# Optimization experiments

Measured on AMD Instinct MI355X. Metric: run time of the kernel, lower is better.

## Reference

```python
import jax, jax.numpy as jnp
import numpy as np

# (npoint, radius, nsample) per SA stage, from module defaults
SA_CFG = [(2048, 0.2, 64), (1024, 0.4, 32), (512, 0.6, 16), (256, 1.2, 8)]


def fps(xyz, npoint):
    """Farthest point sampling, CUDA-kernel semantics: start at index 0.
    xyz: [B,N,3] -> idx [B,npoint] int32."""
    B, N, _ = xyz.shape

    def step(carry, _):
        dist, far = carry
        centroid = jnp.take_along_axis(xyz, far[:, None, None], axis=1)  # [B,1,3]
        d = jnp.sum((xyz - centroid) ** 2, axis=-1)                      # [B,N]
        dist = jnp.minimum(dist, d)
        return (dist, jnp.argmax(dist, axis=-1).astype(jnp.int32)), far

    init = (jnp.full((B, N), 1e10, xyz.dtype), jnp.zeros((B,), jnp.int32))
    _, idxs = jax.lax.scan(step, init, None, length=npoint)  # [npoint,B]
    return idxs.T


def gather(pts, idx):
    """pts: [B,N,C], idx: [B,...] int -> [B,...,C]."""
    return jax.vmap(lambda p, i: p[i])(pts, idx)


def ball_query(xyz, new_xyz, radius, nsample):
    """First-nsample-in-ball semantics of pointnet2 ball_query; pads with the
    first found neighbor. xyz:[B,N,3], new_xyz:[B,S,3] -> [B,S,nsample] int."""
    N = xyz.shape[1]
    # squared dists via ||a||^2 + ||b||^2 - 2ab to avoid a [B,S,N,3] temp
    d2 = (jnp.sum(new_xyz ** 2, -1)[:, :, None]
          + jnp.sum(xyz ** 2, -1)[:, None, :]
          - 2.0 * jnp.einsum('bsc,bnc->bsn', new_xyz, xyz))
    cand = jnp.where(d2 < radius * radius, jnp.arange(N)[None, None, :], N)
    idx = jnp.sort(cand, axis=-1)[..., :nsample]
    first = idx[..., :1]  # center itself is always in the ball (d2==0)
    return jnp.where(idx == N, first, idx)


def sa_stage(xyz, feats, npoint, radius, nsample, layers):
    """One PointnetSAModuleVotes: FPS + ball query + normalized relative xyz
    (use_xyz=True, normalize_xyz=True) + shared MLP + max pool over nsample."""
    fidx = fps(xyz, npoint)
    new_xyz = gather(xyz, fidx)                         # [B,S,3]
    nidx = ball_query(xyz, new_xyz, radius, nsample)    # [B,S,K]
    rel = (gather(xyz, nidx) - new_xyz[:, :, None, :]) / radius  # [B,S,K,3]
    x = rel if feats is None else jnp.concatenate([rel, gather(feats, nidx)], -1)
    for w, b in layers:  # shared 1x1-conv MLP (BN folded), ReLU
        x = jax.nn.relu(x @ w + b)
    return new_xyz, jnp.max(x, axis=2)                  # [B,S,C_out]


def setup_inputs() -> dict:
    key = jax.random.key(0)
    ks = jax.random.split(key, 16)
    inp = {"pointcloud": jax.random.normal(ks[0], (4, 16384, 3), jnp.float32)}
    dims = [(3, 64, 64, 128), (131, 128, 128, 256),
            (259, 256, 256, 512), (515, 512, 512, 512)]
    k = 1
    for s, d in enumerate(dims, 1):
        for l in range(3):
            inp[f"w{s}{l}"] = jax.random.normal(
                jax.random.fold_in(ks[k], l), (d[l], d[l + 1]), jnp.float32) * 0.02
            inp[f"b{s}{l}"] = jnp.zeros((d[l + 1],), jnp.float32)
        k += 1
    return inp


def reference(pointcloud,
              w10, b10, w11, b11, w12, b12,
              w20, b20, w21, b21, w22, b22,
              w30, b30, w31, b31, w32, b32,
              w40, b40, w41, b41, w42, b42):
    stage_params = [
        [(w10, b10), (w11, b11), (w12, b12)],
        [(w20, b20), (w21, b21), (w22, b22)],
        [(w30, b30), (w31, b31), (w32, b32)],
        [(w40, b40), (w41, b41), (w42, b42)],
    ]
    xyz = pointcloud[..., :3]
    feats = None  # input_feature_dim == 0
    for (npoint, radius, nsample), layers in zip(SA_CFG, stage_params):
        xyz, feats = sa_stage(xyz, feats, npoint, radius, nsample, layers)
    return xyz, feats  # sa4_xyz [B,256,3], sa4_features [B,256,512]
```

## Files before the change

### kernel.cpp

```cpp
#include <hip/hip_runtime.h>
#include <hip/hip_bf16.h>


#define B_SZ 4

typedef float v2f __attribute__((ext_vector_type(2)));
typedef unsigned long long u64;

__device__ __forceinline__ v2f pk_add(v2f a, v2f b) {
  v2f d;
  asm("v_pk_add_f32 %0, %1, %2" : "=v"(d) : "v"(a), "v"(b));
  return d;
}
__device__ __forceinline__ v2f pk_mul(v2f a, v2f b) {
  v2f d;
  asm("v_pk_mul_f32 %0, %1, %2" : "=v"(d) : "v"(a), "v"(b));
  return d;
}

template <int CTRL>
__device__ __forceinline__ u64 dpp_u64(u64 v) {
  int lo = (int)(unsigned)v;
  int hi = (int)(unsigned)(v >> 32);
  int nlo = __builtin_amdgcn_update_dpp(lo, lo, CTRL, 0xF, 0xF, false);
  int nhi = __builtin_amdgcn_update_dpp(hi, hi, CTRL, 0xF, 0xF, false);
  return ((u64)(unsigned)nhi << 32) | (unsigned)nlo;
}

__device__ __forceinline__ u64 wave_max_u64(u64 P) {
  u64 o;
  o = dpp_u64<0x111>(P); P = o > P ? o : P;
  o = dpp_u64<0x112>(P); P = o > P ? o : P;
  o = dpp_u64<0x114>(P); P = o > P ? o : P;
  o = dpp_u64<0x118>(P); P = o > P ? o : P;
  o = dpp_u64<0x142>(P); P = o > P ? o : P;
  o = dpp_u64<0x143>(P); P = o > P ? o : P;
  return P;
}

template <int N, int NPOINT, int T>
__global__ __launch_bounds__(T, 2) void fps1_kernel(const float* __restrict__ xyz,
                                                    int* __restrict__ fidx) {
#pragma clang fp contract(off)
  constexpr int PT = N / T;
  static_assert(PT % 2 == 0, "PT even");
  constexpr int NP2 = PT / 2;
  constexpr int NW = T / 64;
  constexpr int NACC = (NP2 >= 4) ? 4 : NP2;
  const int b = blockIdx.x;
  const int t = threadIdx.x;
  const int lane = t & 63;
  const int wv = t >> 6;
  const float* base = xyz + (size_t)b * N * 3;

  v2f px[NP2], py[NP2], pz[NP2], dv[NP2];
  __shared__ __align__(16) u64 s_key[2][NW];
  __shared__ float s_cx[2][NW], s_cy[2][NW], s_cz[2][NW];

#pragma unroll
  for (int j = 0; j < NP2; ++j) {
    int i0 = t + (2 * j) * T;
    int i1 = t + (2 * j + 1) * T;
    px[j][0] = base[i0 * 3 + 0]; py[j][0] = base[i0 * 3 + 1];
    pz[j][0] = base[i0 * 3 + 2];
    px[j][1] = base[i1 * 3 + 0]; py[j][1] = base[i1 * 3 + 1];
    pz[j][1] = base[i1 * 3 + 2];
    dv[j][0] = 1e10f; dv[j][1] = 1e10f;
  }

  int far = 0;
  float cenx = base[0], ceny = base[1], cenz = base[2];
  int p = 0;
  for (int it = 0; it < NPOINT; ++it) {
    if (t == 0) fidx[b * NPOINT + it] = far;
    const float nx = -cenx, ny = -ceny, nz = -cenz;
    const v2f c2x = {nx, nx}, c2y = {ny, ny}, c2z = {nz, nz};

    float mx[NACC];
#pragma unroll
    for (int q = 0; q < NACC; ++q) mx[q] = -1.0f;

#pragma unroll
    for (int j = 0; j < NP2; ++j) {
      v2f dx = pk_add(px[j], c2x);
      v2f dy = pk_add(py[j], c2y);
      v2f dz = pk_add(pz[j], c2z);
      v2f xx = pk_mul(dx, dx);
      v2f yy = pk_mul(dy, dy);
      v2f zz = pk_mul(dz, dz);
      v2f s = pk_add(xx, yy);
      v2f d = pk_add(s, zz);
      float nd0 = fminf(dv[j][0], d[0]);
      float nd1 = fminf(dv[j][1], d[1]);
      dv[j][0] = nd0; dv[j][1] = nd1;
      const int q = j % NACC;
      mx[q] = fmaxf(fmaxf(nd0, nd1), mx[q]);
    }
    float m = mx[0];
#pragma unroll
    for (int q = 1; q < NACC; ++q) m = fmaxf(m, mx[q]);

    int bk = 0;
#pragma unroll
    for (int j = NP2 - 1; j >= 0; --j) {
      if (dv[j][1] == m) bk = 2 * j + 1;
      if (dv[j][0] == m) bk = 2 * j;
    }

    int idx = t + bk * T;
    u64 P = ((u64)__float_as_uint(m) << 32) | (unsigned)(N - idx);
    P = wave_max_u64(P);

    int wf = N - __builtin_amdgcn_readlane((int)(unsigned)(P & 0xffffffffull), 63);
    float wx = base[wf * 3 + 0];
    float wy = base[wf * 3 + 1];
    float wz = base[wf * 3 + 2];
    if (lane == 63) s_key[p][wv] = P;
    if (lane == 0) { s_cx[p][wv] = wx; s_cy[p][wv] = wy; s_cz[p][wv] = wz; }
    __syncthreads();
    u64 bb = s_key[p][0];
    int mw = 0;
#pragma unroll
    for (int w = 1; w < NW; ++w) {
      u64 v = s_key[p][w];
      if (v > bb) { bb = v; mw = w; }
    }
    far = N - (int)(unsigned)(bb & 0xffffffffull);
    cenx = s_cx[p][mw]; ceny = s_cy[p][mw]; cenz = s_cz[p][mw];
    p ^= 1;
  }
}

template <int N, int NPOINT, int T>
__device__ __forceinline__ void fps_body_lds(char* smem,
                                             const float* __restrict__ xyz,
                                             int* __restrict__ fidx, int b) {
#pragma clang fp contract(off)
  constexpr int PT = N / T;
  static_assert(PT % 2 == 0, "PT even");
  constexpr int NP2 = PT / 2;
  constexpr int NW = T / 64;
  constexpr int NACC = (NP2 >= 4) ? 4 : NP2;
  u64* s_pack = (u64*)smem;
  float* s_x = (float*)(smem + 2 * NW * sizeof(u64));
  float* s_y = s_x + N;
  float* s_z = s_y + N;
  const int t = threadIdx.x;
  const int lane = t & 63;
  const int wv = t >> 6;
  const float* base = xyz + (size_t)b * N * 3;

  v2f px[NP2], py[NP2], pz[NP2], dv[NP2];
#pragma unroll
  for (int j = 0; j < NP2; ++j) {
    int i0 = t + (2 * j) * T;
    int i1 = t + (2 * j + 1) * T;
    px[j][0] = base[i0 * 3 + 0]; py[j][0] = base[i0 * 3 + 1];
    pz[j][0] = base[i0 * 3 + 2];
    px[j][1] = base[i1 * 3 + 0]; py[j][1] = base[i1 * 3 + 1];
    pz[j][1] = base[i1 * 3 + 2];
    dv[j][0] = 1e10f; dv[j][1] = 1e10f;
    s_x[i0] = px[j][0]; s_y[i0] = py[j][0]; s_z[i0] = pz[j][0];
    s_x[i1] = px[j][1]; s_y[i1] = py[j][1]; s_z[i1] = pz[j][1];
  }
  __syncthreads();

  int far = 0;
  int p = 0;
  for (int it = 0; it < NPOINT; ++it) {
    if (t == 0) fidx[b * NPOINT + it] = far;
    float cx = s_x[far], cy = s_y[far], cz = s_z[far];
    const float nx = -cx, ny = -cy, nz = -cz;
    const v2f c2x = {nx, nx}, c2y = {ny, ny}, c2z = {nz, nz};

    float mx[NACC];
#pragma unroll
    for (int q = 0; q < NACC; ++q) mx[q] = -1.0f;

#pragma unroll
    for (int j = 0; j < NP2; ++j) {
      v2f dx = pk_add(px[j], c2x);
      v2f dy = pk_add(py[j], c2y);
      v2f dz = pk_add(pz[j], c2z);
      v2f xx = pk_mul(dx, dx);
      v2f yy = pk_mul(dy, dy);
      v2f zz = pk_mul(dz, dz);
      v2f s = pk_add(xx, yy);
      v2f d = pk_add(s, zz);
      float nd0 = fminf(dv[j][0], d[0]);
      float nd1 = fminf(dv[j][1], d[1]);
      dv[j][0] = nd0; dv[j][1] = nd1;
      const int q = j % NACC;
      mx[q] = fmaxf(fmaxf(nd0, nd1), mx[q]);
    }
    float m = mx[0];
#pragma unroll
    for (int q = 1; q < NACC; ++q) m = fmaxf(m, mx[q]);

    int bk = 0;
#pragma unroll
    for (int j = NP2 - 1; j >= 0; --j) {
      if (dv[j][1] == m) bk = 2 * j + 1;
      if (dv[j][0] == m) bk = 2 * j;
    }

    int idx = t + bk * T;
    u64 P = ((u64)__float_as_uint(m) << 32) | (unsigned)(N - idx);
    P = wave_max_u64(P);
    if (lane == 63) s_pack[p * NW + wv] = P;
    __syncthreads();
    u64 bbp = s_pack[p * NW + 0];
#pragma unroll
    for (int w = 1; w < NW; ++w) {
      u64 v = s_pack[p * NW + w];
      bbp = v > bbp ? v : bbp;
    }
    far = N - (int)(unsigned)(bbp & 0xffffffffull);
    p ^= 1;
  }
}

__global__ void gather_xyz_kernel(const float* __restrict__ xyz,
                                  const int* __restrict__ fidx,
                                  float* __restrict__ out, int N, int S) {
  int s = blockIdx.x * blockDim.x + threadIdx.x;
  int b = blockIdx.y;
  if (s < S) {
    int i = fidx[b * S + s];
    out[((size_t)(b * S + s)) * 3 + 0] = xyz[((size_t)(b * N + i)) * 3 + 0];
    out[((size_t)(b * S + s)) * 3 + 1] = xyz[((size_t)(b * N + i)) * 3 + 1];
    out[((size_t)(b * S + s)) * 3 + 2] = xyz[((size_t)(b * N + i)) * 3 + 2];
  }
}

template <int N, int NS>
__global__ __launch_bounds__(256) void ball_query_kernel(
    const float* __restrict__ xyz, const float* __restrict__ new_xyz,
    int* __restrict__ nidx, int S, float r2) {
#pragma clang fp contract(off)
  const int wv = threadIdx.x >> 6;
  const int lane = threadIdx.x & 63;
  const int b = blockIdx.y;
  const int s = blockIdx.x * 4 + wv;
  __shared__ int s_idx[4][NS];
  const float* base = xyz + (size_t)b * N * 3;

  float cx = new_xyz[((size_t)(b * S + s)) * 3 + 0];
  float cy = new_xyz[((size_t)(b * S + s)) * 3 + 1];
  float cz = new_xyz[((size_t)(b * S + s)) * 3 + 2];
  float sc = (cx * cx + cy * cy) + cz * cz;

  int found = 0;
  for (int i0 = 0; i0 < N && found < NS; i0 += 64) {
    int i = i0 + lane;
    float x = base[i * 3 + 0];
    float y = base[i * 3 + 1];
    float z = base[i * 3 + 2];
    float sx = (x * x + y * y) + z * z;
    float dt = (cx * x + cy * y) + cz * z;
    float d2 = (sc + sx) - 2.0f * dt;
    bool inb = d2 < r2;
    unsigned long long m = __ballot(inb);
    if (inb) {
      int pos = found + __popcll(m & ((1ull << lane) - 1));
      if (pos < NS) s_idx[wv][pos] = i;
    }
    found += __popcll(m);
  }
  __syncthreads();
  int fcnt = found < NS ? found : NS;
  int first = s_idx[wv][0];
  int* outp = nidx + ((size_t)(b * S + s)) * NS;
  for (int j = lane; j < NS; j += 64) outp[j] = (j < fcnt) ? s_idx[wv][j] : first;
}

template <int R, int RG, int CG, int CMAXP, int CIN, int COUT>
__device__ __forceinline__ void mlp_layer(float* act, const float* __restrict__ w,
                                          const float* __restrict__ bias, int tid) {
  constexpr int RPT = R / RG;
  constexpr int CPT = COUT / CG;
  static_assert(RG * CG == 256, "thread grid");
  const int rg = tid / CG;
  const int cg = tid % CG;

  float acc[RPT][CPT];
#pragma unroll
  for (int rr = 0; rr < RPT; ++rr)
#pragma unroll
    for (int cc = 0; cc < CPT; ++cc) acc[rr][cc] = 0.f;

  constexpr int K4 = (CIN / 4) * 4;
  for (int k = 0; k < K4; k += 4) {
    float4 a[RPT];
#pragma unroll
    for (int rr = 0; rr < RPT; ++rr)
      a[rr] = *(const float4*)(&act[(rg * RPT + rr) * CMAXP + k]);
    float wvv[4][CPT];
#pragma unroll
    for (int kk = 0; kk < 4; ++kk)
#pragma unroll
      for (int cc = 0; cc < CPT; ++cc)
        wvv[kk][cc] = w[(size_t)(k + kk) * COUT + cg + cc * CG];
#pragma unroll
    for (int rr = 0; rr < RPT; ++rr) {
      float4 av = a[rr];
#pragma unroll
      for (int cc = 0; cc < CPT; ++cc) {
        acc[rr][cc] += av.x * wvv[0][cc];
        acc[rr][cc] += av.y * wvv[1][cc];
        acc[rr][cc] += av.z * wvv[2][cc];
        acc[rr][cc] += av.w * wvv[3][cc];
      }
    }
  }
#pragma unroll 1
  for (int k = K4; k < CIN; ++k) {
    float wvv[CPT];
#pragma unroll
    for (int cc = 0; cc < CPT; ++cc) wvv[cc] = w[(size_t)k * COUT + cg + cc * CG];
#pragma unroll
    for (int rr = 0; rr < RPT; ++rr) {
      float av = act[(rg * RPT + rr) * CMAXP + k];
#pragma unroll
      for (int cc = 0; cc < CPT; ++cc) acc[rr][cc] += av * wvv[cc];
    }
  }
  __syncthreads();
#pragma unroll
  for (int rr = 0; rr < RPT; ++rr)
#pragma unroll
    for (int cc = 0; cc < CPT; ++cc) {
      int co = cg + cc * CG;
      float v = acc[rr][cc] + bias[co];
      act[(rg * RPT + rr) * CMAXP + co] = fmaxf(v, 0.f);
    }
  __syncthreads();
}

template <int NS, int G, int CPREV, int CO0, int CO1, int CO2, int RG, int CG, int CMAXP>
__device__ __forceinline__ void group_mlp_body(
    char* smem, const float* __restrict__ xyz, const float* __restrict__ new_xyz,
    const float* __restrict__ feats, const int* __restrict__ nidx,
    const float* __restrict__ w0, const float* __restrict__ b0,
    const float* __restrict__ w1, const float* __restrict__ b1,
    const float* __restrict__ w2, const float* __restrict__ b2,
    float* __restrict__ out, int N, int S, float radius, int sblk, int b) {
  constexpr int R = NS * G;
  constexpr int CIN = 3 + CPREV;
  float* act = (float*)smem;
  const int tid = threadIdx.x;
  const int s0 = sblk * G;

  for (int i = tid; i < R * CIN; i += 256) {
    int row = i / CIN;
    int ch = i - row * CIN;
    int g = row / NS;
    int j = row - g * NS;
    int sidx = s0 + g;
    int n = nidx[((size_t)(b * S + sidx)) * NS + j];
    float v;
    if constexpr (CPREV == 0) {
      v = (xyz[((size_t)(b * N + n)) * 3 + ch] -
           new_xyz[((size_t)(b * S + sidx)) * 3 + ch]) /
          radius;
    } else {
      if (ch < 3) {
        v = (xyz[((size_t)(b * N + n)) * 3 + ch] -
             new_xyz[((size_t)(b * S + sidx)) * 3 + ch]) /
            radius;
      } else {
        v = feats[((size_t)(b * N + n)) * CPREV + (ch - 3)];
      }
    }
    act[row * CMAXP + ch] = v;
  }
  __syncthreads();

  mlp_layer<R, RG, CG, CMAXP, CIN, CO0>(act, w0, b0, tid);
  mlp_layer<R, RG, CG, CMAXP, CO0, CO1>(act, w1, b1, tid);
  mlp_layer<R, RG, CG, CMAXP, CO1, CO2>(act, w2, b2, tid);

  for (int i = tid; i < G * CO2; i += 256) {
    int g = i / CO2;
    int co = i - g * CO2;
    float m = act[(g * NS) * CMAXP + co];
    for (int j = 1; j < NS; ++j) m = fmaxf(m, act[(g * NS + j) * CMAXP + co]);
    out[((size_t)(b * S + s0 + g)) * CO2 + co] = m;
  }
}

template <int NS, int G, int CPREV, int CO0, int CO1, int CO2, int RG, int CG, int CMAXP>
__global__ __launch_bounds__(256, 4) void group_mlp_kernel(
    const float* __restrict__ xyz, const float* __restrict__ new_xyz,
    const float* __restrict__ feats, const int* __restrict__ nidx,
    const float* __restrict__ w0, const float* __restrict__ b0,
    const float* __restrict__ w1, const float* __restrict__ b1,
    const float* __restrict__ w2, const float* __restrict__ b2,
    float* __restrict__ out, int N, int S, float radius) {
  __shared__ __align__(16) char smem[NS * G * CMAXP * 4];
  group_mlp_body<NS, G, CPREV, CO0, CO1, CO2, RG, CG, CMAXP>(
      smem, xyz, new_xyz, feats, nidx, w0, b0, w1, b1, w2, b2, out, N, S,
      radius, blockIdx.x, blockIdx.y);
}

template <int FN, int FNP, int FT, int NS, int G, int CPREV, int CO0, int CO1,
          int CO2, int RG, int CG, int CMAXP>
__global__ __launch_bounds__(256, 4) void fused_fps_mlp_kernel(
    const float* __restrict__ fpts, int* __restrict__ fidx,
    const float* __restrict__ xyz, const float* __restrict__ new_xyz,
    const float* __restrict__ feats, const int* __restrict__ nidx,
    const float* __restrict__ w0, const float* __restrict__ b0,
    const float* __restrict__ w1, const float* __restrict__ b1,
    const float* __restrict__ w2, const float* __restrict__ b2,
    float* __restrict__ out, int N, int S, float radius, int SBLK) {
  constexpr int FPS_B = 2 * (FT / 64) * (int)sizeof(u64) + 3 * FN * 4;
  constexpr int MLP_B = NS * G * CMAXP * 4;
  constexpr int SB = (FPS_B > MLP_B) ? FPS_B : MLP_B;
  __shared__ __align__(16) char smem[SB];
  if ((int)blockIdx.x < B_SZ) {
    __builtin_amdgcn_s_setprio(1);
    fps_body_lds<FN, FNP, FT>(smem, fpts, fidx, blockIdx.x);
    __builtin_amdgcn_s_setprio(0);
  } else {
    int bid = (int)blockIdx.x - B_SZ;
    group_mlp_body<NS, G, CPREV, CO0, CO1, CO2, RG, CG, CMAXP>(
        smem, xyz, new_xyz, feats, nidx, w0, b0, w1, b1, w2, b2, out, N, S,
        radius, bid % SBLK, bid / SBLK);
  }
}

extern "C" void kernel_launch(void* const* d_in, const int* in_sizes, int n_in,
                              void* d_out, int out_size, void* d_ws, size_t ws_size,
                              hipStream_t stream) {
  (void)in_sizes; (void)n_in; (void)out_size; (void)ws_size;
  const float* pc = (const float*)d_in[0];
  const float* W[4][3];
  const float* Bb[4][3];
  for (int s = 0; s < 4; ++s)
    for (int l = 0; l < 3; ++l) {
      W[s][l] = (const float*)d_in[1 + s * 6 + l * 2];
      Bb[s][l] = (const float*)d_in[2 + s * 6 + l * 2];
    }

  char* wsp = (char*)d_ws;
  int* fidx = (int*)wsp;
  int* nidx = (int*)(wsp + (32 << 10));
  float* xyzA = (float*)(wsp + (32 << 10) + (2 << 20));
  float* xyzB = xyzA + B_SZ * 2048 * 3;
  float* featA = xyzB + B_SZ * 2048 * 3;
  float* featB = featA + B_SZ * 2048 * 128;
  float* oxyz = (float*)d_out;
  float* ofeat = oxyz + B_SZ * 256 * 3;

  hipLaunchKernelGGL((fps1_kernel<16384, 2048, 512>), dim3(B_SZ), dim3(512), 0, stream,
                     pc, fidx);
  hipLaunchKernelGGL(gather_xyz_kernel, dim3(32, B_SZ), dim3(64), 0, stream,
                     pc, fidx, xyzA, 16384, 2048);
  hipLaunchKernelGGL((ball_query_kernel<16384, 64>), dim3(512, B_SZ), dim3(256), 0, stream,
                     pc, xyzA, nidx, 2048, (float)(0.2 * 0.2));

  hipLaunchKernelGGL((fused_fps_mlp_kernel<2048, 1024, 256,
                                           64, 1, 0, 64, 64, 128, 8, 32, 128>),
                     dim3(B_SZ + 2048 * B_SZ), dim3(256), 0, stream,
                     xyzA, fidx,
                     pc, xyzA, (const float*)nullptr, nidx,
                     W[0][0], Bb[0][0], W[0][1], Bb[0][1], W[0][2], Bb[0][2],
                     featA, 16384, 2048, 0.2f, 2048);
  hipLaunchKernelGGL(gather_xyz_kernel, dim3(16, B_SZ), dim3(64), 0, stream,
                     xyzA, fidx, xyzB, 2048, 1024);
  hipLaunchKernelGGL((ball_query_kernel<2048, 32>), dim3(256, B_SZ), dim3(256), 0, stream,
                     xyzA, xyzB, nidx, 1024, (float)(0.4 * 0.4));

  hipLaunchKernelGGL((fused_fps_mlp_kernel<1024, 512, 256,
                                           32, 1, 128, 128, 128, 256, 4, 64, 256>),
                     dim3(B_SZ + 1024 * B_SZ), dim3(256), 0, stream,
                     xyzB, fidx,
                     xyzA, xyzB, featA, nidx,
                     W[1][0], Bb[1][0], W[1][1], Bb[1][1], W[1][2], Bb[1][2],
                     featB, 2048, 1024, 0.4f, 1024);
  hipLaunchKernelGGL(gather_xyz_kernel, dim3(8, B_SZ), dim3(64), 0, stream,
                     xyzB, fidx, xyzA, 1024, 512);
  hipLaunchKernelGGL((ball_query_kernel<1024, 16>), dim3(128, B_SZ), dim3(256), 0, stream,
                     xyzB, xyzA, nidx, 512, (float)(0.6 * 0.6));

  hipLaunchKernelGGL((fused_fps_mlp_kernel<512, 256, 256,
                                           16, 1, 256, 256, 256, 512, 2, 128, 512>),
                     dim3(B_SZ + 512 * B_SZ), dim3(256), 0, stream,
                     xyzA, fidx,
                     xyzB, xyzA, featB, nidx,
                     W[2][0], Bb[2][0], W[2][1], Bb[2][1], W[2][2], Bb[2][2],
                     featA, 1024, 512, 0.6f, 512);
  hipLaunchKernelGGL(gather_xyz_kernel, dim3(4, B_SZ), dim3(64), 0, stream,
                     xyzA, fidx, oxyz, 512, 256);
  hipLaunchKernelGGL((ball_query_kernel<512, 8>), dim3(64, B_SZ), dim3(256), 0, stream,
                     xyzA, oxyz, nidx, 256, (float)(1.2 * 1.2));

  hipLaunchKernelGGL((group_mlp_kernel<8, 2, 512, 512, 512, 512, 2, 128, 516>),
                     dim3(128, B_SZ), dim3(256), 0, stream,
                     xyzA, oxyz, featA, nidx,
                     W[3][0], Bb[3][0], W[3][1], Bb[3][1], W[3][2], Bb[3][2],
                     ofeat, 512, 256, 1.2f);
}
```

Baseline: 5.031 ms.

## Run stage 2-4 FPS in a single wave without block barriers

The later-stage FPS loops, which share a kernel with the grouped MLP, now run on one 64-lane wave instead of a 256-thread block. Each iteration finishes with a wave-level DPP reduction and a readlane, with no __syncthreads or LDS exchange. Points are kept in LDS as float4 so the next centroid comes from one load. The stage-1 FPS now fetches the winning centroid from global memory after the block reduction instead of passing per-wave candidates through LDS, and the index rescan is split into independent chunks. The trade is more registers and serial work per lane in the single-wave version, plus a dependent global load per iteration in stage 1.

```diff
diff --git a/kernel.cpp b/kernel.cpp
--- a/kernel.cpp
+++ b/kernel.cpp
@@ -38,15 +38,68 @@
   return P;
 }
 
+template <int NP2>
+__device__ __forceinline__ float upd_pts(const v2f* px, const v2f* py,
+                                         const v2f* pz, v2f* dv, float cx,
+                                         float cy, float cz) {
+#pragma clang fp contract(off)
+  constexpr int NACC = (NP2 >= 4) ? 4 : NP2;
+  const float nx = -cx, ny = -cy, nz = -cz;
+  const v2f c2x = {nx, nx}, c2y = {ny, ny}, c2z = {nz, nz};
+  float mx[NACC];
+#pragma unroll
+  for (int q = 0; q < NACC; ++q) mx[q] = -1.0f;
+#pragma unroll
+  for (int j = 0; j < NP2; ++j) {
+    v2f dx = pk_add(px[j], c2x);
+    v2f dy = pk_add(py[j], c2y);
+    v2f dz = pk_add(pz[j], c2z);
+    v2f xx = pk_mul(dx, dx);
+    v2f yy = pk_mul(dy, dy);
+    v2f zz = pk_mul(dz, dz);
+    v2f s = pk_add(xx, yy);
+    v2f d = pk_add(s, zz);
+    float nd0 = fminf(dv[j][0], d[0]);
+    float nd1 = fminf(dv[j][1], d[1]);
+    dv[j][0] = nd0; dv[j][1] = nd1;
+    const int q = j % NACC;
+    mx[q] = fmaxf(fmaxf(nd0, nd1), mx[q]);
+  }
+  float m = mx[0];
+#pragma unroll
+  for (int q = 1; q < NACC; ++q) m = fmaxf(m, mx[q]);
+  return m;
+}
+
+template <int NP2>
+__device__ __forceinline__ int rescan_idx(const v2f* dv, float m) {
+  constexpr int NCH = (NP2 >= 4) ? 4 : NP2;
+  constexpr int CL = NP2 / NCH;
+  int bkq[NCH];
+#pragma unroll
+  for (int q = 0; q < NCH; ++q) {
+    int bk = 0x7fffffff;
+#pragma unroll
+    for (int jj = CL - 1; jj >= 0; --jj) {
+      int j = q * CL + jj;
+      if (dv[j][1] == m) bk = 2 * j + 1;
+      if (dv[j][0] == m) bk = 2 * j;
+    }
+    bkq[q] = bk;
+  }
+  int bk = bkq[NCH - 1];
+#pragma unroll
+  for (int q = NCH - 2; q >= 0; --q) bk = (bkq[q] != 0x7fffffff) ? bkq[q] : bk;
+  return bk;
+}
+
 template <int N, int NPOINT, int T>
 __global__ __launch_bounds__(T, 2) void fps1_kernel(const float* __restrict__ xyz,
                                                     int* __restrict__ fidx) {
 #pragma clang fp contract(off)
   constexpr int PT = N / T;
-  static_assert(PT % 2 == 0, "PT even");
   constexpr int NP2 = PT / 2;
   constexpr int NW = T / 64;
-  constexpr int NACC = (NP2 >= 4) ? 4 : NP2;
   const int b = blockIdx.x;
   const int t = threadIdx.x;
   const int lane = t & 63;
@@ -54,8 +107,7 @@
   const float* base = xyz + (size_t)b * N * 3;
 
   v2f px[NP2], py[NP2], pz[NP2], dv[NP2];
-  __shared__ __align__(16) u64 s_key[2][NW];
-  __shared__ float s_cx[2][NW], s_cy[2][NW], s_cz[2][NW];
+  __shared__ __align__(16) u64 s_pack[2][NW];
 
 #pragma unroll
   for (int j = 0; j < NP2; ++j) {
@@ -73,150 +125,64 @@
   int p = 0;
   for (int it = 0; it < NPOINT; ++it) {
     if (t == 0) fidx[b * NPOINT + it] = far;
-    const float nx = -cenx, ny = -ceny, nz = -cenz;
-    const v2f c2x = {nx, nx}, c2y = {ny, ny}, c2z = {nz, nz};
-
-    float mx[NACC];
-#pragma unroll
-    for (int q = 0; q < NACC; ++q) mx[q] = -1.0f;
-
-#pragma unroll
-    for (int j = 0; j < NP2; ++j) {
-      v2f dx = pk_add(px[j], c2x);
-      v2f dy = pk_add(py[j], c2y);
-      v2f dz = pk_add(pz[j], c2z);
-      v2f xx = pk_mul(dx, dx);
-      v2f yy = pk_mul(dy, dy);
-      v2f zz = pk_mul(dz, dz);
-      v2f s = pk_add(xx, yy);
-      v2f d = pk_add(s, zz);
-      float nd0 = fminf(dv[j][0], d[0]);
-      float nd1 = fminf(dv[j][1], d[1]);
-      dv[j][0] = nd0; dv[j][1] = nd1;
-      const int q = j % NACC;
-      mx[q] = fmaxf(fmaxf(nd0, nd1), mx[q]);
-    }
-    float m = mx[0];
-#pragma unroll
-    for (int q = 1; q < NACC; ++q) m = fmaxf(m, mx[q]);
-
-    int bk = 0;
-#pragma unroll
-    for (int j = NP2 - 1; j >= 0; --j) {
-      if (dv[j][1] == m) bk = 2 * j + 1;
-      if (dv[j][0] == m) bk = 2 * j;
-    }
-
+    float m = upd_pts<NP2>(px, py, pz, dv, cenx, ceny, cenz);
+    int bk = rescan_idx<NP2>(dv, m);
     int idx = t + bk * T;
     u64 P = ((u64)__float_as_uint(m) << 32) | (unsigned)(N - idx);
     P = wave_max_u64(P);
-
-    int wf = N - __builtin_amdgcn_readlane((int)(unsigned)(P & 0xffffffffull), 63);
-    float wx = base[wf * 3 + 0];
-    float wy = base[wf * 3 + 1];
-    float wz = base[wf * 3 + 2];
-    if (lane == 63) s_key[p][wv] = P;
-    if (lane == 0) { s_cx[p][wv] = wx; s_cy[p][wv] = wy; s_cz[p][wv] = wz; }
+    if (lane == 63) s_pack[p][wv] = P;
     __syncthreads();
-    u64 bb = s_key[p][0];
-    int mw = 0;
+    u64 bb = s_pack[p][0];
 #pragma unroll
     for (int w = 1; w < NW; ++w) {
-      u64 v = s_key[p][w];
-      if (v > bb) { bb = v; mw = w; }
+      u64 v = s_pack[p][w];
+      bb = v > bb ? v : bb;
     }
     far = N - (int)(unsigned)(bb & 0xffffffffull);
-    cenx = s_cx[p][mw]; ceny = s_cy[p][mw]; cenz = s_cz[p][mw];
+    cenx = base[far * 3 + 0];
+    ceny = base[far * 3 + 1];
+    cenz = base[far * 3 + 2];
     p ^= 1;
   }
 }
 
-template <int N, int NPOINT, int T>
-__device__ __forceinline__ void fps_body_lds(char* smem,
-                                             const float* __restrict__ xyz,
-                                             int* __restrict__ fidx, int b) {
+template <int N, int NPOINT>
+__device__ __forceinline__ void fps_wave_body(char* smem,
+                                              const float* __restrict__ xyz,
+                                              int* __restrict__ fidx, int b) {
 #pragma clang fp contract(off)
-  constexpr int PT = N / T;
-  static_assert(PT % 2 == 0, "PT even");
+  constexpr int PT = N / 64;
   constexpr int NP2 = PT / 2;
-  constexpr int NW = T / 64;
-  constexpr int NACC = (NP2 >= 4) ? 4 : NP2;
-  u64* s_pack = (u64*)smem;
-  float* s_x = (float*)(smem + 2 * NW * sizeof(u64));
-  float* s_y = s_x + N;
-  float* s_z = s_y + N;
-  const int t = threadIdx.x;
-  const int lane = t & 63;
-  const int wv = t >> 6;
+  float4* s_p = (float4*)smem;
+  const int lane = threadIdx.x & 63;
   const float* base = xyz + (size_t)b * N * 3;
 
   v2f px[NP2], py[NP2], pz[NP2], dv[NP2];
 #pragma unroll
   for (int j = 0; j < NP2; ++j) {
-    int i0 = t + (2 * j) * T;
-    int i1 = t + (2 * j + 1) * T;
-    px[j][0] = base[i0 * 3 + 0]; py[j][0] = base[i0 * 3 + 1];
-    pz[j][0] = base[i0 * 3 + 2];
-    px[j][1] = base[i1 * 3 + 0]; py[j][1] = base[i1 * 3 + 1];
-    pz[j][1] = base[i1 * 3 + 2];
+    int i0 = lane + (2 * j) * 64;
+    int i1 = lane + (2 * j + 1) * 64;
+    float x0 = base[i0 * 3 + 0], y0 = base[i0 * 3 + 1], z0 = base[i0 * 3 + 2];
+    float x1 = base[i1 * 3 + 0], y1 = base[i1 * 3 + 1], z1 = base[i1 * 3 + 2];
+    px[j][0] = x0; py[j][0] = y0; pz[j][0] = z0;
+    px[j][1] = x1; py[j][1] = y1; pz[j][1] = z1;
     dv[j][0] = 1e10f; dv[j][1] = 1e10f;
-    s_x[i0] = px[j][0]; s_y[i0] = py[j][0]; s_z[i0] = pz[j][0];
-    s_x[i1] = px[j][1]; s_y[i1] = py[j][1]; s_z[i1] = pz[j][1];
-  }
-  __syncthreads();
+    s_p[i0] = make_float4(x0, y0, z0, 0.f);
+    s_p[i1] = make_float4(x1, y1, z1, 0.f);
+  }
+  asm volatile("s_waitcnt lgkmcnt(0)" ::: "memory");
 
   int far = 0;
-  int p = 0;
+  float4 cen = s_p[0];
   for (int it = 0; it < NPOINT; ++it) {
-    if (t == 0) fidx[b * NPOINT + it] = far;
-    float cx = s_x[far], cy = s_y[far], cz = s_z[far];
-    const float nx = -cx, ny = -cy, nz = -cz;
-    const v2f c2x = {nx, nx}, c2y = {ny, ny}, c2z = {nz, nz};
-
-    float mx[NACC];
-#pragma unroll
-    for (int q = 0; q < NACC; ++q) mx[q] = -1.0f;
-
-#pragma unroll
-    for (int j = 0; j < NP2; ++j) {
-      v2f dx = pk_add(px[j], c2x);
-      v2f dy = pk_add(py[j], c2y);
-      v2f dz = pk_add(pz[j], c2z);
-      v2f xx = pk_mul(dx, dx);
-      v2f yy = pk_mul(dy, dy);
-      v2f zz = pk_mul(dz, dz);
-      v2f s = pk_add(xx, yy);
-      v2f d = pk_add(s, zz);
-      float nd0 = fminf(dv[j][0], d[0]);
-      float nd1 = fminf(dv[j][1], d[1]);
-      dv[j][0] = nd0; dv[j][1] = nd1;
-      const int q = j % NACC;
-      mx[q] = fmaxf(fmaxf(nd0, nd1), mx[q]);
-    }
-    float m = mx[0];
-#pragma unroll
-    for (int q = 1; q < NACC; ++q) m = fmaxf(m, mx[q]);
-
-    int bk = 0;
-#pragma unroll
-    for (int j = NP2 - 1; j >= 0; --j) {
-      if (dv[j][1] == m) bk = 2 * j + 1;
-      if (dv[j][0] == m) bk = 2 * j;
-    }
-
-    int idx = t + bk * T;
+    if (lane == 0) fidx[b * NPOINT + it] = far;
+    float m = upd_pts<NP2>(px, py, pz, dv, cen.x, cen.y, cen.z);
+    int bk = rescan_idx<NP2>(dv, m);
+    int idx = lane + bk * 64;
     u64 P = ((u64)__float_as_uint(m) << 32) | (unsigned)(N - idx);
     P = wave_max_u64(P);
-    if (lane == 63) s_pack[p * NW + wv] = P;
-    __syncthreads();
-    u64 bbp = s_pack[p * NW + 0];
-#pragma unroll
-    for (int w = 1; w < NW; ++w) {
-      u64 v = s_pack[p * NW + w];
-      bbp = v > bbp ? v : bbp;
-    }
-    far = N - (int)(unsigned)(bbp & 0xffffffffull);
-    p ^= 1;
+    far = N - __builtin_amdgcn_readlane((int)(unsigned)(P & 0xffffffffull), 63);
+    cen = s_p[far];
   }
 }
 
@@ -403,7 +369,7 @@
       radius, blockIdx.x, blockIdx.y);
 }
 
-template <int FN, int FNP, int FT, int NS, int G, int CPREV, int CO0, int CO1,
+template <int FN, int FNP, int NS, int G, int CPREV, int CO0, int CO1,
           int CO2, int RG, int CG, int CMAXP>
 __global__ __launch_bounds__(256, 4) void fused_fps_mlp_kernel(
     const float* __restrict__ fpts, int* __restrict__ fidx,
@@ -413,14 +379,16 @@
     const float* __restrict__ w1, const float* __restrict__ b1,
     const float* __restrict__ w2, const float* __restrict__ b2,
     float* __restrict__ out, int N, int S, float radius, int SBLK) {
-  constexpr int FPS_B = 2 * (FT / 64) * (int)sizeof(u64) + 3 * FN * 4;
+  constexpr int FPS_B = FN * 16;
   constexpr int MLP_B = NS * G * CMAXP * 4;
   constexpr int SB = (FPS_B > MLP_B) ? FPS_B : MLP_B;
   __shared__ __align__(16) char smem[SB];
   if ((int)blockIdx.x < B_SZ) {
-    __builtin_amdgcn_s_setprio(1);
-    fps_body_lds<FN, FNP, FT>(smem, fpts, fidx, blockIdx.x);
-    __builtin_amdgcn_s_setprio(0);
+    if (threadIdx.x < 64) {
+      __builtin_amdgcn_s_setprio(1);
+      fps_wave_body<FN, FNP>(smem, fpts, fidx, blockIdx.x);
+      __builtin_amdgcn_s_setprio(0);
+    }
   } else {
     int bid = (int)blockIdx.x - B_SZ;
     group_mlp_body<NS, G, CPREV, CO0, CO1, CO2, RG, CG, CMAXP>(
@@ -459,7 +427,7 @@
   hipLaunchKernelGGL((ball_query_kernel<16384, 64>), dim3(512, B_SZ), dim3(256), 0, stream,
                      pc, xyzA, nidx, 2048, (float)(0.2 * 0.2));
 
-  hipLaunchKernelGGL((fused_fps_mlp_kernel<2048, 1024, 256,
+  hipLaunchKernelGGL((fused_fps_mlp_kernel<2048, 1024,
                                            64, 1, 0, 64, 64, 128, 8, 32, 128>),
                      dim3(B_SZ + 2048 * B_SZ), dim3(256), 0, stream,
                      xyzA, fidx,
@@ -471,7 +439,7 @@
   hipLaunchKernelGGL((ball_query_kernel<2048, 32>), dim3(256, B_SZ), dim3(256), 0, stream,
                      xyzA, xyzB, nidx, 1024, (float)(0.4 * 0.4));
 
-  hipLaunchKernelGGL((fused_fps_mlp_kernel<1024, 512, 256,
+  hipLaunchKernelGGL((fused_fps_mlp_kernel<1024, 512,
                                            32, 1, 128, 128, 128, 256, 4, 64, 256>),
                      dim3(B_SZ + 1024 * B_SZ), dim3(256), 0, stream,
                      xyzB, fidx,
@@ -483,7 +451,7 @@
   hipLaunchKernelGGL((ball_query_kernel<1024, 16>), dim3(128, B_SZ), dim3(256), 0, stream,
                      xyzB, xyzA, nidx, 512, (float)(0.6 * 0.6));
 
-  hipLaunchKernelGGL((fused_fps_mlp_kernel<512, 256, 256,
+  hipLaunchKernelGGL((fused_fps_mlp_kernel<512, 256,
                                            16, 1, 256, 256, 256, 512, 2, 128, 512>),
                      dim3(B_SZ + 512 * B_SZ), dim3(256), 0, stream,
                      xyzA, fidx,
```

Measured after the change: 5.576 ms. 1.11x slower.
